# Performance work log

Measured on AMD Instinct MI355X. Metric: run time of the kernel, lower is better.

## Reference

```python
import jax, jax.numpy as jnp
import numpy as np

HIDDEN = 4096
N_HEADS = 32
N_KV_HEADS = 8
HEAD_DIM = HIDDEN // N_HEADS  # 128
Q_SIZE = N_HEADS * HEAD_DIM
KV_SIZE = N_KV_HEADS * HEAD_DIM
ROPE_THETA = 10000.0
EPS = 1e-5
SCALE = HEAD_DIM ** -0.5


def _headwise_layernorm(x, weight, eps):
    # x: [B,S,H,D], weight: [H,D]; LayerNorm over last dim (head_dim), fp32 math
    xf = x.astype(jnp.float32)
    mean = xf.mean(-1, keepdims=True)
    var = jnp.square(xf - mean).mean(-1, keepdims=True)
    y = (xf - mean) * jax.lax.rsqrt(var + eps)
    return (weight.astype(jnp.float32) * y).astype(x.dtype)


def _rope_gptj(x, positions):
    # non-neox (GPT-J) style: rotate interleaved pairs. x: [B,S,H,D]
    half = HEAD_DIM // 2
    inv_freq = 1.0 / (ROPE_THETA ** (jnp.arange(0, HEAD_DIM, 2, dtype=jnp.float32) / HEAD_DIM))
    ang = positions.astype(jnp.float32)[..., None] * inv_freq  # [B,S,half]
    cos = jnp.cos(ang)[:, :, None, :]  # [B,S,1,half]
    sin = jnp.sin(ang)[:, :, None, :]
    x1 = x[..., 0::2]
    x2 = x[..., 1::2]
    o1 = x1 * cos - x2 * sin
    o2 = x2 * cos + x1 * sin
    # re-interleave
    out = jnp.stack([o1, o2], axis=-1).reshape(x.shape)
    return out.astype(x.dtype)


def setup_inputs() -> dict:
    key = jax.random.key(0)
    k1, k2, k3, k4 = jax.random.split(key, 4)
    B, S = 2, 2048
    positions = jnp.tile(jnp.arange(S, dtype=jnp.int32)[None, :], (B, 1))
    hidden_states = jax.random.normal(k1, (B, S, HIDDEN), dtype=jnp.float32)
    Wqkv = jax.random.normal(k2, (HIDDEN, Q_SIZE + 2 * KV_SIZE), dtype=jnp.float32) * (HIDDEN ** -0.5)
    Wo = jax.random.normal(k3, (Q_SIZE, HIDDEN), dtype=jnp.float32) * (Q_SIZE ** -0.5)
    kq, kk = jax.random.split(k4)
    q_norm_w = jnp.ones((N_HEADS, HEAD_DIM), jnp.float32) + 0.02 * jax.random.normal(kq, (N_HEADS, HEAD_DIM))
    k_norm_w = jnp.ones((N_KV_HEADS, HEAD_DIM), jnp.float32) + 0.02 * jax.random.normal(kk, (N_KV_HEADS, HEAD_DIM))
    return {"positions": positions, "hidden_states": hidden_states, "Wqkv": Wqkv,
            "q_norm_w": q_norm_w, "k_norm_w": k_norm_w, "Wo": Wo}


def reference(positions, hidden_states, Wqkv, q_norm_w, k_norm_w, Wo):
    B, S, _ = hidden_states.shape
    qkv = hidden_states @ Wqkv  # [B,S,Q+2KV]
    q, k, v = jnp.split(qkv, [Q_SIZE, Q_SIZE + KV_SIZE], axis=-1)
    q = q.reshape(B, S, N_HEADS, HEAD_DIM)
    k = k.reshape(B, S, N_KV_HEADS, HEAD_DIM)
    v = v.reshape(B, S, N_KV_HEADS, HEAD_DIM)
    # per-head qk-norm
    q = _headwise_layernorm(q, q_norm_w, EPS)
    k = _headwise_layernorm(k, k_norm_w, EPS)
    # non-neox RoPE
    q = _rope_gptj(q, positions)
    k = _rope_gptj(k, positions)
    # GQA: repeat kv heads
    n_rep = N_HEADS // N_KV_HEADS
    k = jnp.repeat(k, n_rep, axis=2)  # [B,S,H,D]
    v = jnp.repeat(v, n_rep, axis=2)
    scores = jnp.einsum('bqhd,bkhd->bhqk', q, k) * SCALE
    causal = jnp.tril(jnp.ones((S, S), dtype=bool))
    scores = jnp.where(causal[None, None], scores, jnp.finfo(scores.dtype).min)
    probs = jax.nn.softmax(scores, axis=-1)
    attn = jnp.einsum('bhqk,bkhd->bqhd', probs, v).reshape(B, S, Q_SIZE)
    return attn @ Wo
```

## Files before the change

kernel.cpp:

```cpp
#include <hip/hip_runtime.h>
#include <hip/hip_bf16.h>
#include <cstdint>

typedef unsigned short u16;
typedef unsigned int u32;
typedef __attribute__((ext_vector_type(8))) short bf16x8;
typedef __attribute__((ext_vector_type(4))) float f32x4;
typedef __attribute__((ext_vector_type(16))) float f32x16;
typedef __attribute__((ext_vector_type(4))) unsigned int u32x4;

#define HIDDEN 4096
#define NH 32
#define NKV 8
#define HD 128
#define QSZ 4096
#define KVSZ 1024
#define QKV_N 6144
#define SEQ 2048
#define NB 2
#define NTOK (NB*SEQ)
#define ATT_SCALE 0.08838834764831845f
#define LOG2E 1.4426950408889634f
#define LN_EPS 1e-5f
#define THRD 12.0f

__device__ __forceinline__ u16 f2bf(float f) {
  union { float f; u32 u; } a; a.f = f;
  u32 r = a.u + 0x7fffu + ((a.u >> 16) & 1u);
  return (u16)(r >> 16);
}
__device__ __forceinline__ float bf2f(u16 h) {
  union { u32 u; float f; } a; a.u = ((u32)h) << 16;
  return a.f;
}

__device__ __forceinline__ void gload_lds16(const void* g, void* l) {
  __builtin_amdgcn_global_load_lds(
      (const __attribute__((address_space(1))) void*)g,
      (__attribute__((address_space(3))) void*)l,
      16, 0, 0);
}

__global__ __launch_bounds__(256)
void conv_f32_bf16(const float* __restrict__ in, u16* __restrict__ out, int n8) {
  int i = blockIdx.x * 256 + threadIdx.x;
  if (i >= n8) return;
  const float4* p = (const float4*)in + (size_t)i * 2;
  float4 v0 = p[0], v1 = p[1];
  u32x4 o;
  o.x = (u32)f2bf(v0.x) | ((u32)f2bf(v0.y) << 16);
  o.y = (u32)f2bf(v0.z) | ((u32)f2bf(v0.w) << 16);
  o.z = (u32)f2bf(v1.x) | ((u32)f2bf(v1.y) << 16);
  o.w = (u32)f2bf(v1.z) | ((u32)f2bf(v1.w) << 16);
  ((u32x4*)out)[i] = o;
}

__global__ __launch_bounds__(256)
void transp_f32_bf16(const float* __restrict__ in, u16* __restrict__ out, int R, int C) {
  __shared__ float tile[32][33];
  int c0 = blockIdx.x << 5, r0 = blockIdx.y << 5;
  int tx = threadIdx.x & 31, ty = threadIdx.x >> 5;
  #pragma unroll
  for (int j = 0; j < 32; j += 8)
    tile[ty + j][tx] = in[(long)(r0 + ty + j) * C + c0 + tx];
  __syncthreads();
  #pragma unroll
  for (int j = 0; j < 32; j += 8)
    out[(long)(c0 + ty + j) * R + r0 + tx] = f2bf(tile[tx][ty + j]);
}

template<typename OutT>
__global__ __launch_bounds__(512, 2)
void gemm_bt6(const u16* __restrict__ A, const u16* __restrict__ Bt,
              OutT* __restrict__ C, int N, int K) {
  extern __shared__ char smem[];
  const int t = threadIdx.x;
  const int lane = t & 63, w = t >> 6;
  const int wr = w >> 2, wc = w & 3;
  const int l31 = lane & 31, l7 = lane & 7, g2 = lane >> 5;
  const int bm = blockIdx.y, bn = blockIdx.x;

  const int ciA0 = t, ciA1 = t + 512;
  const u16* AgS0 = A + (long)(bm * 128 + (ciA0 >> 3)) * K + (((ciA0 & 7) ^ ((ciA0 >> 3) & 7)) << 3);
  const u16* AgS1 = A + (long)(bm * 128 + (ciA1 >> 3)) * K + (((ciA1 & 7) ^ ((ciA1 >> 3) & 7)) << 3);
  const u16* BgS0;
  const u16* BgS1;
  const u16* BgS2;
  const u16* BgS3;
  {
    int ci0 = t, ci1 = t + 512, ci2 = t + 1024, ci3 = t + 1536;
    BgS0 = Bt + (long)(bn * 256 + (ci0 >> 3)) * K + (((ci0 & 7) ^ ((ci0 >> 3) & 7)) << 3);
    BgS1 = Bt + (long)(bn * 256 + (ci1 >> 3)) * K + (((ci1 & 7) ^ ((ci1 >> 3) & 7)) << 3);
    BgS2 = Bt + (long)(bn * 256 + (ci2 >> 3)) * K + (((ci2 & 7) ^ ((ci2 >> 3) & 7)) << 3);
    BgS3 = Bt + (long)(bn * 256 + (ci3 >> 3)) * K + (((ci3 & 7) ^ ((ci3 >> 3) & 7)) << 3);
  }
  const int dA0 = (w * 64) * 16;
  const int dA1 = (512 + w * 64) * 16;
  const int dB0 = 16384 + (w * 64) * 16;
  const int dB1 = 16384 + (512 + w * 64) * 16;
  const int dB2 = 16384 + (1024 + w * 64) * 16;
  const int dB3 = 16384 + (1536 + w * 64) * 16;

  const int arow0 = (wr * 64 + l31) * 128;
  const int brow0 = 16384 + (wc * 64 + l31) * 128;

  f32x16 acc[2][2];
  #pragma unroll
  for (int i = 0; i < 2; ++i)
    #pragma unroll
    for (int j = 0; j < 2; ++j)
      #pragma unroll
      for (int r = 0; r < 16; ++r) acc[i][j][r] = 0.f;

  const int nt = K >> 6;
  char* cbase = smem;
  char* nbase = smem + 49152;
  char* sbase = smem + 98304;

  #define STAGE6(dst, koff) { \
    gload_lds16(AgS0 + (koff), dst + dA0);  gload_lds16(AgS1 + (koff), dst + dA1); \
    gload_lds16(BgS0 + (koff), dst + dB0);  gload_lds16(BgS1 + (koff), dst + dB1); \
    gload_lds16(BgS2 + (koff), dst + dB2);  gload_lds16(BgS3 + (koff), dst + dB3); }

  STAGE6(cbase, 0);
  STAGE6(nbase, 64);
  asm volatile("s_waitcnt vmcnt(6)" ::: "memory");
  __builtin_amdgcn_s_barrier();
  __builtin_amdgcn_sched_barrier(0);

  #define READ_KK(dst, kkv) { \
    const int pcb = (((kkv) * 2 + g2) ^ l7) * 16; \
    dst[0] = *(const bf16x8*)(cbase + arow0 + pcb); \
    dst[1] = *(const bf16x8*)(cbase + arow0 + 32 * 128 + pcb); \
    dst[2] = *(const bf16x8*)(cbase + brow0 + pcb); \
    dst[3] = *(const bf16x8*)(cbase + brow0 + 32 * 128 + pcb); }
  #define MFMA_KK(f) { \
    __builtin_amdgcn_s_setprio(1); \
    acc[0][0] = __builtin_amdgcn_mfma_f32_32x32x16_bf16(f[0], f[2], acc[0][0], 0, 0, 0); \
    acc[0][1] = __builtin_amdgcn_mfma_f32_32x32x16_bf16(f[0], f[3], acc[0][1], 0, 0, 0); \
    acc[1][0] = __builtin_amdgcn_mfma_f32_32x32x16_bf16(f[1], f[2], acc[1][0], 0, 0, 0); \
    acc[1][1] = __builtin_amdgcn_mfma_f32_32x32x16_bf16(f[1], f[3], acc[1][1], 0, 0, 0); \
    __builtin_amdgcn_s_setprio(0); }

  for (int tt = 0; tt < nt; ++tt) {
    const long sk = (long)((tt + 2 < nt) ? (tt + 2) : (nt - 1)) * 64;
    STAGE6(sbase, sk);
    bf16x8 fA[4], fB[4], fC[4], fD[4];
    READ_KK(fA, 0);
    READ_KK(fB, 1);
    MFMA_KK(fA);
    READ_KK(fC, 2);
    MFMA_KK(fB);
    READ_KK(fD, 3);
    MFMA_KK(fC);
    MFMA_KK(fD);
    asm volatile("s_waitcnt vmcnt(6)" ::: "memory");
    __builtin_amdgcn_s_barrier();
    __builtin_amdgcn_sched_barrier(0);
    char* tmp = cbase; cbase = nbase; nbase = sbase; sbase = tmp;
  }
  #undef READ_KK
  #undef MFMA_KK
  #undef STAGE6

  #pragma unroll
  for (int mf = 0; mf < 2; ++mf)
    #pragma unroll
    for (int nf = 0; nf < 2; ++nf)
      #pragma unroll
      for (int r = 0; r < 16; ++r) {
        long row = bm * 128 + wr * 64 + mf * 32 + (r & 3) + 8 * (r >> 2) + 4 * g2;
        long col = bn * 256 + wc * 64 + nf * 32 + l31;
        float v = acc[mf][nf][r];
        if constexpr (sizeof(OutT) == 2) C[row * N + col] = f2bf(v);
        else                             C[row * N + col] = v;
      }
}

__device__ __forceinline__ void ln_rope_head(const u16* __restrict__ src,
                                             const float* __restrict__ wgt,
                                             u16* __restrict__ dst,
                                             int lane, float sa, float ca, float scale) {
  u32 xr = *(const u32*)(src + 2 * lane);
  float x1 = bf2f((u16)(xr & 0xffffu)), x2 = bf2f((u16)(xr >> 16));
  float ssum = x1 + x2;
  #pragma unroll
  for (int off = 1; off < 64; off <<= 1) ssum += __shfl_xor(ssum, off);
  float mean = ssum * (1.0f / 128.0f);
  float e1 = x1 - mean, e2 = x2 - mean;
  float vv = e1 * e1 + e2 * e2;
  #pragma unroll
  for (int off = 1; off < 64; off <<= 1) vv += __shfl_xor(vv, off);
  float rstd = rsqrtf(vv * (1.0f / 128.0f) + LN_EPS);
  float y1 = e1 * rstd * wgt[2 * lane];
  float y2 = e2 * rstd * wgt[2 * lane + 1];
  float o1 = (y1 * ca - y2 * sa) * scale;
  float o2 = (y2 * ca + y1 * sa) * scale;
  *(u32*)(dst + 2 * lane) = (u32)f2bf(o1) | ((u32)f2bf(o2) << 16);
}

__global__ __launch_bounds__(512)
void ln_rope(const u16* __restrict__ qkv, const int* __restrict__ pos,
             const float* __restrict__ qw, const float* __restrict__ kw,
             u16* __restrict__ qo, u16* __restrict__ ko) {
  const int s = blockIdx.x, b = blockIdx.y;
  const int t = threadIdx.x, lane = t & 63, w = t >> 6;
  const long base = (long)(b * SEQ + s) * QKV_N;
  const int p = pos[b * SEQ + s];
  const float expo = (float)(2 * lane) * (1.0f / 128.0f);
  const float inv_freq = exp2f(-expo * 13.287712379549449f);
  float sa, ca;
  sincosf((float)p * inv_freq, &sa, &ca);
  #pragma unroll
  for (int hh = 0; hh < 4; ++hh) {
    int h = w + hh * 8;
    ln_rope_head(qkv + base + h * HD, qw + h * HD,
                 qo + (((long)b * NH + h) * SEQ + s) * HD, lane, sa, ca,
                 ATT_SCALE * LOG2E);
  }
  ln_rope_head(qkv + base + QSZ + w * HD, kw + w * HD,
               ko + (((long)b * NKV + w) * SEQ + s) * HD, lane, sa, ca, 1.0f);
}

__global__ __launch_bounds__(256)
void v_transp(const u16* __restrict__ qkv, u16* __restrict__ vt) {
  __shared__ u16 tile[32][33];
  int s0 = blockIdx.x * 32, d0 = blockIdx.y * 32;
  int bk = blockIdx.z;
  int b = bk >> 3, kvh = bk & 7;
  int tx = threadIdx.x & 31, ty = threadIdx.x >> 5;
  const u16* src = qkv + ((long)(b * SEQ) + s0) * QKV_N + QSZ + KVSZ + kvh * HD + d0;
  #pragma unroll
  for (int j = 0; j < 32; j += 8)
    tile[ty + j][tx] = src[(long)(ty + j) * QKV_N + tx];
  __syncthreads();
  u16* dst = vt + (((long)bk) * HD + d0) * SEQ + s0;
  #pragma unroll
  for (int j = 0; j < 32; j += 8)
    dst[(long)(ty + j) * SEQ + tx] = tile[tx][ty + j];
}

__global__ __launch_bounds__(512, 2)
void flash_attn2(const u16* __restrict__ Qg, const u16* __restrict__ Kg,
                 const u16* __restrict__ Vtg, u16* __restrict__ Og) {
  const int lin = blockIdx.x;
  const int b = lin >> 8;
  const int rem = lin & 255;
  const int h = rem >> 3;
  const int q3 = rem & 7;
  const int qt = b ? (7 - q3) : q3;
  const int kvh = h >> 2;
  const int t = threadIdx.x, lane = t & 63, w = t >> 6;
  const int hh = lane >> 5, l31 = lane & 31;
  const int wq0 = qt * 256 + w * 32;
  const int q = wq0 + l31;

  __shared__ u16 Klds[2][64 * 128];
  __shared__ u16 Vlds[2][128 * 64];

  const u16* Qbase = Qg + (((long)b * NH + h) * SEQ + q) * HD + hh * 8;
  bf16x8 qf[8];
  #pragma unroll
  for (int ks = 0; ks < 8; ++ks) qf[ks] = *(const bf16x8*)(Qbase + ks * 16);

  f32x16 o[4];
  #pragma unroll
  for (int i = 0; i < 4; ++i)
    #pragma unroll
    for (int r = 0; r < 16; ++r) o[i][r] = 0.f;
  float m = -1e30f, l = 0.f;

  const u16* Kbase = Kg + ((long)b * NKV + kvh) * (long)SEQ * HD;
  const u16* Vtbase = Vtg + ((long)b * NKV + kvh) * (long)HD * SEQ;
  const int nt = qt * 4 + 4;

  auto STAGE = [&](int buf, int kt) {
    const int kv0 = kt * 64;
    #pragma unroll
    for (int i = 0; i < 2; ++i) {
      int c = t + i * 512;
      int kv = c >> 4, cc = c & 15;
      int cl = (cc & 8) | ((cc ^ kv) & 7);
      gload_lds16(Kbase + (long)(kv0 + kv) * HD + cl * 8,
                  (char*)(&Klds[buf][0]) + (i * 512 + w * 64) * 16);
    }
    #pragma unroll
    for (int i = 0; i < 2; ++i) {
      int c = t + i * 512;
      int d = c >> 3, cc = c & 7;
      int cl = cc ^ (d & 7);
      gload_lds16(Vtbase + (long)d * SEQ + kv0 + cl * 8,
                  (char*)(&Vlds[buf][0]) + (i * 512 + w * 64) * 16);
    }
  };

  STAGE(0, 0);
  __syncthreads();
  int cur = 0;
  for (int kt = 0; kt < nt; ++kt) {
    const int kv0 = kt * 64;
    if (kt + 1 < nt) STAGE(cur ^ 1, kt + 1);
    if (kv0 <= wq0 + 31) {
      const char* Kb = (const char*)(&Klds[cur][0]);
      const char* Vb = (const char*)(&Vlds[cur][0]);
      f32x16 st[2];
      #pragma unroll
      for (int tt = 0; tt < 2; ++tt)
        #pragma unroll
        for (int r = 0; r < 16; ++r) st[tt][r] = 0.f;
      __builtin_amdgcn_s_setprio(1);
      #pragma unroll
      for (int tt = 0; tt < 2; ++tt) {
        if (kv0 + tt * 32 <= wq0 + 31) {
          #pragma unroll
          for (int ks = 0; ks < 8; ++ks) {
            int ch = ks * 2 + hh;
            int pc = (ch & 8) | ((ch ^ l31) & 7);
            bf16x8 kf = *(const bf16x8*)(Kb + (tt * 32 + l31) * 256 + pc * 16);
            st[tt] = __builtin_amdgcn_mfma_f32_32x32x16_bf16(kf, qf[ks], st[tt], 0, 0, 0);
          }
        }
      }
      __builtin_amdgcn_s_setprio(0);
      if (kv0 + 63 > wq0) {
        #pragma unroll
        for (int tt = 0; tt < 2; ++tt)
          #pragma unroll
          for (int r = 0; r < 16; ++r) {
            int kva = kv0 + tt * 32 + (r & 3) + 8 * (r >> 2) + 4 * hh;
            if (kva > q) st[tt][r] = -1e30f;
          }
      }
      float p0 = -1e30f, p1 = -1e30f, p2 = -1e30f, p3 = -1e30f;
      #pragma unroll
      for (int tt = 0; tt < 2; ++tt)
        #pragma unroll
        for (int r = 0; r < 16; r += 4) {
          p0 = fmaxf(p0, st[tt][r]);
          p1 = fmaxf(p1, st[tt][r + 1]);
          p2 = fmaxf(p2, st[tt][r + 2]);
          p3 = fmaxf(p3, st[tt][r + 3]);
        }
      float mx = fmaxf(fmaxf(p0, p1), fmaxf(p2, p3));
      mx = fmaxf(mx, __shfl_xor(mx, 32));
      if (!__all(mx - m <= THRD)) {
        float mn = fmaxf(m, mx);
        float sc = exp2f(m - mn);
        m = mn;
        float scr[16];
        #pragma unroll
        for (int r = 0; r < 16; ++r)
          scr[r] = __shfl(sc, (r & 3) + 8 * (r >> 2) + 4 * hh);
        #pragma unroll
        for (int db = 0; db < 4; ++db)
          #pragma unroll
          for (int r = 0; r < 16; ++r) o[db][r] *= scr[r];
        l *= sc;
      }
      float s0 = 0.f, s1 = 0.f, s2 = 0.f, s3 = 0.f;
      #pragma unroll
      for (int tt = 0; tt < 2; ++tt)
        #pragma unroll
        for (int r = 0; r < 16; r += 4) {
          float e0 = exp2f(st[tt][r] - m);
          float e1 = exp2f(st[tt][r + 1] - m);
          float e2 = exp2f(st[tt][r + 2] - m);
          float e3 = exp2f(st[tt][r + 3] - m);
          st[tt][r] = e0; st[tt][r + 1] = e1; st[tt][r + 2] = e2; st[tt][r + 3] = e3;
          s0 += e0; s1 += e1; s2 += e2; s3 += e3;
        }
      float rs = (s0 + s1) + (s2 + s3);
      rs += __shfl_xor(rs, 32);
      l += rs;
      bf16x8 pa[4];
      #pragma unroll
      for (int k4 = 0; k4 < 4; ++k4) {
        int s8 = (k4 & 1) * 8, tt = k4 >> 1;
        u32 x0 = (u32)f2bf(st[tt][s8 + 0]) | ((u32)f2bf(st[tt][s8 + 1]) << 16);
        u32 x1 = (u32)f2bf(st[tt][s8 + 2]) | ((u32)f2bf(st[tt][s8 + 3]) << 16);
        u32 y0 = (u32)f2bf(st[tt][s8 + 4]) | ((u32)f2bf(st[tt][s8 + 5]) << 16);
        u32 y1 = (u32)f2bf(st[tt][s8 + 6]) | ((u32)f2bf(st[tt][s8 + 7]) << 16);
        u32 x0s = (u32)__shfl_xor((int)x0, 32), x1s = (u32)__shfl_xor((int)x1, 32);
        u32 y0s = (u32)__shfl_xor((int)y0, 32), y1s = (u32)__shfl_xor((int)y1, 32);
        union { u32 u[4]; bf16x8 v; } pk;
        pk.u[0] = hh ? y0s : x0;
        pk.u[1] = hh ? y1s : x1;
        pk.u[2] = hh ? y0 : x0s;
        pk.u[3] = hh ? y1 : x1s;
        pa[k4] = pk.v;
      }
      __builtin_amdgcn_s_setprio(1);
      #pragma unroll
      for (int k4 = 0; k4 < 4; ++k4)
        #pragma unroll
        for (int db = 0; db < 4; ++db) {
          int ch = k4 * 2 + hh;
          int pcc = ch ^ (l31 & 7);
          bf16x8 vf = *(const bf16x8*)(Vb + (db * 32 + l31) * 128 + pcc * 16);
          o[db] = __builtin_amdgcn_mfma_f32_32x32x16_bf16(pa[k4], vf, o[db], 0, 0, 0);
        }
      __builtin_amdgcn_s_setprio(0);
    }
    __syncthreads();
    cur ^= 1;
  }
  float linv = 1.0f / l;
  float li[16];
  #pragma unroll
  for (int r = 0; r < 16; ++r)
    li[r] = __shfl(linv, (r & 3) + 8 * (r >> 2) + 4 * hh);
  #pragma unroll
  for (int db = 0; db < 4; ++db)
    #pragma unroll
    for (int r = 0; r < 16; ++r) {
      int qr = wq0 + (r & 3) + 8 * (r >> 2) + 4 * hh;
      Og[((long)b * SEQ + qr) * QSZ + h * HD + db * 32 + l31] = f2bf(o[db][r] * li[r]);
    }
}

extern "C" void kernel_launch(void* const* d_in, const int* in_sizes, int n_in,
                              void* d_out, int out_size, void* d_ws, size_t ws_size,
                              hipStream_t stream) {
  const int*   positions = (const int*)d_in[0];
  const float* hidden    = (const float*)d_in[1];
  const float* Wqkv      = (const float*)d_in[2];
  const float* qnw       = (const float*)d_in[3];
  const float* knw       = (const float*)d_in[4];
  const float* Wo        = (const float*)d_in[5];
  float* out = (float*)d_out;
  char* ws = (char*)d_ws;
  const size_t MB = 1024 * 1024;
  u16* hbf   = (u16*)(ws + 0);
  u16* WqkvT = (u16*)(ws + 32 * MB);
  u16* qkvb  = (u16*)(ws + 80 * MB);
  u16* q_arr = (u16*)(ws + 0);
  u16* k_arr = (u16*)(ws + 32 * MB);
  u16* vt_arr= (u16*)(ws + 40 * MB);
  u16* WoT   = (u16*)(ws + 48 * MB);
  u16* Oarr  = (u16*)(ws + 80 * MB);

  const int GEMM_LDS = 3 * 49152;
  (void)hipFuncSetAttribute((const void*)&gemm_bt6<u16>,
        hipFuncAttributeMaxDynamicSharedMemorySize, GEMM_LDS);
  (void)hipFuncSetAttribute((const void*)&gemm_bt6<float>,
        hipFuncAttributeMaxDynamicSharedMemorySize, GEMM_LDS);

  conv_f32_bf16<<<dim3(NTOK * HIDDEN / 8 / 256), 256, 0, stream>>>(hidden, hbf, NTOK * HIDDEN / 8);
  transp_f32_bf16<<<dim3(QKV_N / 32, HIDDEN / 32), 256, 0, stream>>>(Wqkv, WqkvT, HIDDEN, QKV_N);
  gemm_bt6<u16><<<dim3(QKV_N / 256, NTOK / 128), 512, GEMM_LDS, stream>>>(hbf, WqkvT, qkvb, QKV_N, HIDDEN);
  ln_rope<<<dim3(SEQ, NB), 512, 0, stream>>>(qkvb, positions, qnw, knw, q_arr, k_arr);
  v_transp<<<dim3(SEQ / 32, HD / 32, NB * NKV), 256, 0, stream>>>(qkvb, vt_arr);
  transp_f32_bf16<<<dim3(HIDDEN / 32, QSZ / 32), 256, 0, stream>>>(Wo, WoT, QSZ, HIDDEN);
  flash_attn2<<<dim3(512), 512, 0, stream>>>(q_arr, k_arr, vt_arr, Oarr);
  gemm_bt6<float><<<dim3(HIDDEN / 256, NTOK / 128), 512, GEMM_LDS, stream>>>(Oarr, WoT, out, HIDDEN, QSZ);
}
```

Baseline: 584.7 us.

## Halve GEMM K-step for higher occupancy and pair causal query tiles in attention

```diff
diff --git a/kernel.cpp b/kernel.cpp
--- a/kernel.cpp
+++ b/kernel.cpp
@@ -70,39 +70,33 @@
 }
 
 template<typename OutT>
-__global__ __launch_bounds__(512, 2)
-void gemm_bt6(const u16* __restrict__ A, const u16* __restrict__ Bt,
+__global__ __launch_bounds__(512, 4)
+void gemm_bt9(const u16* __restrict__ A, const u16* __restrict__ Bt,
               OutT* __restrict__ C, int N, int K) {
   extern __shared__ char smem[];
   const int t = threadIdx.x;
   const int lane = t & 63, w = t >> 6;
   const int wr = w >> 2, wc = w & 3;
-  const int l31 = lane & 31, l7 = lane & 7, g2 = lane >> 5;
+  const int l31 = lane & 31, g2 = lane >> 5;
   const int bm = blockIdx.y, bn = blockIdx.x;
 
-  const int ciA0 = t, ciA1 = t + 512;
-  const u16* AgS0 = A + (long)(bm * 128 + (ciA0 >> 3)) * K + (((ciA0 & 7) ^ ((ciA0 >> 3) & 7)) << 3);
-  const u16* AgS1 = A + (long)(bm * 128 + (ciA1 >> 3)) * K + (((ciA1 & 7) ^ ((ciA1 >> 3) & 7)) << 3);
-  const u16* BgS0;
-  const u16* BgS1;
-  const u16* BgS2;
-  const u16* BgS3;
+  const u16* pA;  const u16* pB0;  const u16* pB1;
   {
-    int ci0 = t, ci1 = t + 512, ci2 = t + 1024, ci3 = t + 1536;
-    BgS0 = Bt + (long)(bn * 256 + (ci0 >> 3)) * K + (((ci0 & 7) ^ ((ci0 >> 3) & 7)) << 3);
-    BgS1 = Bt + (long)(bn * 256 + (ci1 >> 3)) * K + (((ci1 & 7) ^ ((ci1 >> 3) & 7)) << 3);
-    BgS2 = Bt + (long)(bn * 256 + (ci2 >> 3)) * K + (((ci2 & 7) ^ ((ci2 >> 3) & 7)) << 3);
-    BgS3 = Bt + (long)(bn * 256 + (ci3 >> 3)) * K + (((ci3 & 7) ^ ((ci3 >> 3) & 7)) << 3);
+    int ci = t;
+    int line = ci >> 3, phys = ci & 7;
+    int lg = phys ^ (line & 7);
+    pA = A + (long)(bm * 128 + 2 * line + (lg >> 2)) * K + ((lg & 3) << 3);
+    ci = t;
+    line = ci >> 3; phys = ci & 7; lg = phys ^ (line & 7);
+    pB0 = Bt + (long)(bn * 256 + 2 * line + (lg >> 2)) * K + ((lg & 3) << 3);
+    ci = t + 512;
+    line = ci >> 3; phys = ci & 7; lg = phys ^ (line & 7);
+    pB1 = Bt + (long)(bn * 256 + 2 * line + (lg >> 2)) * K + ((lg & 3) << 3);
   }
-  const int dA0 = (w * 64) * 16;
-  const int dA1 = (512 + w * 64) * 16;
-  const int dB0 = 16384 + (w * 64) * 16;
-  const int dB1 = 16384 + (512 + w * 64) * 16;
-  const int dB2 = 16384 + (1024 + w * 64) * 16;
-  const int dB3 = 16384 + (1536 + w * 64) * 16;
-
-  const int arow0 = (wr * 64 + l31) * 128;
-  const int brow0 = 16384 + (wc * 64 + l31) * 128;
+  const int dS = w * 1024;
+
+  const int lhalf = l31 >> 1;
+  const int lgbase = (l31 & 1) * 4 + g2;
 
   f32x16 acc[2][2];
   #pragma unroll
@@ -112,29 +106,33 @@
       #pragma unroll
       for (int r = 0; r < 16; ++r) acc[i][j][r] = 0.f;
 
-  const int nt = K >> 6;
+  const int nt = K >> 5;
   char* cbase = smem;
-  char* nbase = smem + 49152;
-  char* sbase = smem + 98304;
-
-  #define STAGE6(dst, koff) { \
-    gload_lds16(AgS0 + (koff), dst + dA0);  gload_lds16(AgS1 + (koff), dst + dA1); \
-    gload_lds16(BgS0 + (koff), dst + dB0);  gload_lds16(BgS1 + (koff), dst + dB1); \
-    gload_lds16(BgS2 + (koff), dst + dB2);  gload_lds16(BgS3 + (koff), dst + dB3); }
-
-  STAGE6(cbase, 0);
-  STAGE6(nbase, 64);
-  asm volatile("s_waitcnt vmcnt(6)" ::: "memory");
+  char* nbase = smem + 24576;
+  char* sbase = smem + 49152;
+
+  #define STAGE9(dst, koff) { \
+    gload_lds16(pA  + (koff), (dst) + dS); \
+    gload_lds16(pB0 + (koff), (dst) + 8192 + dS); \
+    gload_lds16(pB1 + (koff), (dst) + 16384 + dS); }
+
+  STAGE9(cbase, 0);
+  STAGE9(nbase, 32);
+  asm volatile("s_waitcnt vmcnt(3)" ::: "memory");
   __builtin_amdgcn_s_barrier();
   __builtin_amdgcn_sched_barrier(0);
 
-  #define READ_KK(dst, kkv) { \
-    const int pcb = (((kkv) * 2 + g2) ^ l7) * 16; \
-    dst[0] = *(const bf16x8*)(cbase + arow0 + pcb); \
-    dst[1] = *(const bf16x8*)(cbase + arow0 + 32 * 128 + pcb); \
-    dst[2] = *(const bf16x8*)(cbase + brow0 + pcb); \
-    dst[3] = *(const bf16x8*)(cbase + brow0 + 32 * 128 + pcb); }
-  #define MFMA_KK(f) { \
+  #define READ9(dst, s) { \
+    const int lg_ = lgbase + (s) * 2; \
+    { int ln_ = wr * 32 + lhalf;          int ph_ = lg_ ^ (ln_ & 7); \
+      dst[0] = *(const bf16x8*)(cbase + ln_ * 128 + ph_ * 16); } \
+    { int ln_ = wr * 32 + 16 + lhalf;     int ph_ = lg_ ^ (ln_ & 7); \
+      dst[1] = *(const bf16x8*)(cbase + ln_ * 128 + ph_ * 16); } \
+    { int ln_ = wc * 32 + lhalf;          int ph_ = lg_ ^ (ln_ & 7); \
+      dst[2] = *(const bf16x8*)(cbase + 8192 + ln_ * 128 + ph_ * 16); } \
+    { int ln_ = wc * 32 + 16 + lhalf;     int ph_ = lg_ ^ (ln_ & 7); \
+      dst[3] = *(const bf16x8*)(cbase + 8192 + ln_ * 128 + ph_ * 16); } }
+  #define MFMA9(f) { \
     __builtin_amdgcn_s_setprio(1); \
     acc[0][0] = __builtin_amdgcn_mfma_f32_32x32x16_bf16(f[0], f[2], acc[0][0], 0, 0, 0); \
     acc[0][1] = __builtin_amdgcn_mfma_f32_32x32x16_bf16(f[0], f[3], acc[0][1], 0, 0, 0); \
@@ -143,25 +141,21 @@
     __builtin_amdgcn_s_setprio(0); }
 
   for (int tt = 0; tt < nt; ++tt) {
-    const long sk = (long)((tt + 2 < nt) ? (tt + 2) : (nt - 1)) * 64;
-    STAGE6(sbase, sk);
-    bf16x8 fA[4], fB[4], fC[4], fD[4];
-    READ_KK(fA, 0);
-    READ_KK(fB, 1);
-    MFMA_KK(fA);
-    READ_KK(fC, 2);
-    MFMA_KK(fB);
-    READ_KK(fD, 3);
-    MFMA_KK(fC);
-    MFMA_KK(fD);
-    asm volatile("s_waitcnt vmcnt(6)" ::: "memory");
+    const long sk = (long)((tt + 2 < nt) ? (tt + 2) : (nt - 1)) * 32;
+    bf16x8 f0[4], f1[4];
+    READ9(f0, 0);
+    READ9(f1, 1);
+    STAGE9(sbase, sk);
+    MFMA9(f0);
+    MFMA9(f1);
+    asm volatile("s_waitcnt vmcnt(3)" ::: "memory");
     __builtin_amdgcn_s_barrier();
     __builtin_amdgcn_sched_barrier(0);
     char* tmp = cbase; cbase = nbase; nbase = sbase; sbase = tmp;
   }
-  #undef READ_KK
-  #undef MFMA_KK
-  #undef STAGE6
+  #undef READ9
+  #undef MFMA9
+  #undef STAGE9
 
   #pragma unroll
   for (int mf = 0; mf < 2; ++mf)
@@ -241,38 +235,22 @@
 }
 
 __global__ __launch_bounds__(512, 2)
-void flash_attn2(const u16* __restrict__ Qg, const u16* __restrict__ Kg,
+void flash_attn3(const u16* __restrict__ Qg, const u16* __restrict__ Kg,
                  const u16* __restrict__ Vtg, u16* __restrict__ Og) {
   const int lin = blockIdx.x;
-  const int b = lin >> 8;
-  const int rem = lin & 255;
-  const int h = rem >> 3;
-  const int q3 = rem & 7;
-  const int qt = b ? (7 - q3) : q3;
+  const int b = lin >> 7;
+  const int rem = lin & 127;
+  const int h = rem >> 2;
+  const int qp = rem & 3;
   const int kvh = h >> 2;
   const int t = threadIdx.x, lane = t & 63, w = t >> 6;
   const int hh = lane >> 5, l31 = lane & 31;
-  const int wq0 = qt * 256 + w * 32;
-  const int q = wq0 + l31;
 
   __shared__ u16 Klds[2][64 * 128];
   __shared__ u16 Vlds[2][128 * 64];
 
-  const u16* Qbase = Qg + (((long)b * NH + h) * SEQ + q) * HD + hh * 8;
-  bf16x8 qf[8];
-  #pragma unroll
-  for (int ks = 0; ks < 8; ++ks) qf[ks] = *(const bf16x8*)(Qbase + ks * 16);
-
-  f32x16 o[4];
-  #pragma unroll
-  for (int i = 0; i < 4; ++i)
-    #pragma unroll
-    for (int r = 0; r < 16; ++r) o[i][r] = 0.f;
-  float m = -1e30f, l = 0.f;
-
   const u16* Kbase = Kg + ((long)b * NKV + kvh) * (long)SEQ * HD;
   const u16* Vtbase = Vtg + ((long)b * NKV + kvh) * (long)HD * SEQ;
-  const int nt = qt * 4 + 4;
 
   auto STAGE = [&](int buf, int kt) {
     const int kv0 = kt * 64;
@@ -294,128 +272,147 @@
     }
   };
 
-  STAGE(0, 0);
-  __syncthreads();
-  int cur = 0;
-  for (int kt = 0; kt < nt; ++kt) {
-    const int kv0 = kt * 64;
-    if (kt + 1 < nt) STAGE(cur ^ 1, kt + 1);
-    if (kv0 <= wq0 + 31) {
-      const char* Kb = (const char*)(&Klds[cur][0]);
-      const char* Vb = (const char*)(&Vlds[cur][0]);
-      f32x16 st[2];
+  for (int seg = 0; seg < 2; ++seg) {
+    const int qt = seg ? qp : (7 - qp);
+    const int wq0 = qt * 256 + w * 32;
+    const int q = wq0 + l31;
+    const u16* Qbase = Qg + (((long)b * NH + h) * SEQ + q) * HD + hh * 8;
+    bf16x8 qf[8];
+    #pragma unroll
+    for (int ks = 0; ks < 8; ++ks) qf[ks] = *(const bf16x8*)(Qbase + ks * 16);
+
+    f32x16 o[4];
+    #pragma unroll
+    for (int i = 0; i < 4; ++i)
       #pragma unroll
-      for (int tt = 0; tt < 2; ++tt)
-        #pragma unroll
-        for (int r = 0; r < 16; ++r) st[tt][r] = 0.f;
-      __builtin_amdgcn_s_setprio(1);
-      #pragma unroll
-      for (int tt = 0; tt < 2; ++tt) {
-        if (kv0 + tt * 32 <= wq0 + 31) {
-          #pragma unroll
-          for (int ks = 0; ks < 8; ++ks) {
-            int ch = ks * 2 + hh;
-            int pc = (ch & 8) | ((ch ^ l31) & 7);
-            bf16x8 kf = *(const bf16x8*)(Kb + (tt * 32 + l31) * 256 + pc * 16);
-            st[tt] = __builtin_amdgcn_mfma_f32_32x32x16_bf16(kf, qf[ks], st[tt], 0, 0, 0);
+      for (int r = 0; r < 16; ++r) o[i][r] = 0.f;
+    float m = -1e30f, l = 0.f;
+    const int nt = qt * 4 + 4;
+
+    __syncthreads();
+    STAGE(0, 0);
+    __syncthreads();
+    int cur = 0;
+    for (int kt = 0; kt < nt; ++kt) {
+      const int kv0 = kt * 64;
+      if (kt + 1 < nt) STAGE(cur ^ 1, kt + 1);
+      if (kv0 <= wq0 + 31) {
+        const char* Kb = (const char*)(&Klds[cur][0]);
+        const char* Vb = (const char*)(&Vlds[cur][0]);
+        f32x16 st[2];
+        #pragma unroll
+        for (int tt = 0; tt < 2; ++tt)
+          #pragma unroll
+          for (int r = 0; r < 16; ++r) st[tt][r] = 0.f;
+        __builtin_amdgcn_s_setprio(1);
+        #pragma unroll
+        for (int tt = 0; tt < 2; ++tt) {
+          if (kv0 + tt * 32 <= wq0 + 31) {
+            #pragma unroll
+            for (int ks = 0; ks < 8; ++ks) {
+              int ch = ks * 2 + hh;
+              int pc = (ch & 8) | ((ch ^ l31) & 7);
+              bf16x8 kf = *(const bf16x8*)(Kb + (tt * 32 + l31) * 256 + pc * 16);
+              st[tt] = __builtin_amdgcn_mfma_f32_32x32x16_bf16(kf, qf[ks], st[tt], 0, 0, 0);
+            }
           }
         }
+        __builtin_amdgcn_s_setprio(0);
+        if (kv0 + 63 > wq0) {
+          #pragma unroll
+          for (int tt = 0; tt < 2; ++tt)
+            #pragma unroll
+            for (int r = 0; r < 16; ++r) {
+              int kva = kv0 + tt * 32 + (r & 3) + 8 * (r >> 2) + 4 * hh;
+              if (kva > q) st[tt][r] = -1e30f;
+            }
+        }
+        float p0 = -1e30f, p1 = -1e30f, p2 = -1e30f, p3 = -1e30f;
+        #pragma unroll
+        for (int tt = 0; tt < 2; ++tt)
+          #pragma unroll
+          for (int r = 0; r < 16; r += 4) {
+            p0 = fmaxf(p0, st[tt][r]);
+            p1 = fmaxf(p1, st[tt][r + 1]);
+            p2 = fmaxf(p2, st[tt][r + 2]);
+            p3 = fmaxf(p3, st[tt][r + 3]);
+          }
+        float mx = fmaxf(fmaxf(p0, p1), fmaxf(p2, p3));
+        mx = fmaxf(mx, __shfl_xor(mx, 32));
+        if (!__all(mx - m <= THRD)) {
+          float mn = fmaxf(m, mx);
+          float sc = exp2f(m - mn);
+          m = mn;
+          float scr[16];
+          #pragma unroll
+          for (int r = 0; r < 16; ++r)
+            scr[r] = __shfl(sc, (r & 3) + 8 * (r >> 2) + 4 * hh);
+          #pragma unroll
+          for (int db = 0; db < 4; ++db)
+            #pragma unroll
+            for (int r = 0; r < 16; ++r) o[db][r] *= scr[r];
+          l *= sc;
+        }
+        float s0 = 0.f, s1 = 0.f, s2 = 0.f, s3 = 0.f;
+        #pragma unroll
+        for (int tt = 0; tt < 2; ++tt)
+          #pragma unroll
+          for (int r = 0; r < 16; r += 4) {
+            float e0 = exp2f(st[tt][r] - m);
+            float e1 = exp2f(st[tt][r + 1] - m);
+            float e2 = exp2f(st[tt][r + 2] - m);
+            float e3 = exp2f(st[tt][r + 3] - m);
+            st[tt][r] = e0; st[tt][r + 1] = e1; st[tt][r + 2] = e2; st[tt][r + 3] = e3;
+            s0 += e0; s1 += e1; s2 += e2; s3 += e3;
+          }
+        float rs = (s0 + s1) + (s2 + s3);
+        rs += __shfl_xor(rs, 32);
+        l += rs;
+        bf16x8 pa[4];
+        #pragma unroll
+        for (int k4 = 0; k4 < 4; ++k4) {
+          int s8 = (k4 & 1) * 8, tt = k4 >> 1;
+          u32 x0 = (u32)f2bf(st[tt][s8 + 0]) | ((u32)f2bf(st[tt][s8 + 1]) << 16);
+          u32 x1 = (u32)f2bf(st[tt][s8 + 2]) | ((u32)f2bf(st[tt][s8 + 3]) << 16);
+          u32 y0 = (u32)f2bf(st[tt][s8 + 4]) | ((u32)f2bf(st[tt][s8 + 5]) << 16);
+          u32 y1 = (u32)f2bf(st[tt][s8 + 6]) | ((u32)f2bf(st[tt][s8 + 7]) << 16);
+          u32 x0s = (u32)__shfl_xor((int)x0, 32), x1s = (u32)__shfl_xor((int)x1, 32);
+          u32 y0s = (u32)__shfl_xor((int)y0, 32), y1s = (u32)__shfl_xor((int)y1, 32);
+          union { u32 u[4]; bf16x8 v; } pk;
+          pk.u[0] = hh ? y0s : x0;
+          pk.u[1] = hh ? y1s : x1;
+          pk.u[2] = hh ? y0 : x0s;
+          pk.u[3] = hh ? y1 : x1s;
+          pa[k4] = pk.v;
+        }
+        __builtin_amdgcn_s_setprio(1);
+        #pragma unroll
+        for (int k4 = 0; k4 < 4; ++k4)
+          #pragma unroll
+          for (int db = 0; db < 4; ++db) {
+            int ch = k4 * 2 + hh;
+            int pcc = ch ^ (l31 & 7);
+            bf16x8 vf = *(const bf16x8*)(Vb + (db * 32 + l31) * 128 + pcc * 16);
+            o[db] = __builtin_amdgcn_mfma_f32_32x32x16_bf16(pa[k4], vf, o[db], 0, 0, 0);
+          }
+        __builtin_amdgcn_s_setprio(0);
       }
-      __builtin_amdgcn_s_setprio(0);
-      if (kv0 + 63 > wq0) {
-        #pragma unroll
-        for (int tt = 0; tt < 2; ++tt)
-          #pragma unroll
-          for (int r = 0; r < 16; ++r) {
-            int kva = kv0 + tt * 32 + (r & 3) + 8 * (r >> 2) + 4 * hh;
-            if (kva > q) st[tt][r] = -1e30f;
-          }
+      __syncthreads();
+      cur ^= 1;
+    }
+    float linv = 1.0f / l;
+    float li[16];
+    #pragma unroll
+    for (int r = 0; r < 16; ++r)
+      li[r] = __shfl(linv, (r & 3) + 8 * (r >> 2) + 4 * hh);
+    #pragma unroll
+    for (int db = 0; db < 4; ++db)
+      #pragma unroll
+      for (int r = 0; r < 16; ++r) {
+        int qr = wq0 + (r & 3) + 8 * (r >> 2) + 4 * hh;
+        Og[((long)b * SEQ + qr) * QSZ + h * HD + db * 32 + l31] = f2bf(o[db][r] * li[r]);
       }
-      float p0 = -1e30f, p1 = -1e30f, p2 = -1e30f, p3 = -1e30f;
-      #pragma unroll
-      for (int tt = 0; tt < 2; ++tt)
-        #pragma unroll
-        for (int r = 0; r < 16; r += 4) {
-          p0 = fmaxf(p0, st[tt][r]);
-          p1 = fmaxf(p1, st[tt][r + 1]);
-          p2 = fmaxf(p2, st[tt][r + 2]);
-          p3 = fmaxf(p3, st[tt][r + 3]);
-        }
-      float mx = fmaxf(fmaxf(p0, p1), fmaxf(p2, p3));
-      mx = fmaxf(mx, __shfl_xor(mx, 32));
-      if (!__all(mx - m <= THRD)) {
-        float mn = fmaxf(m, mx);
-        float sc = exp2f(m - mn);
-        m = mn;
-        float scr[16];
-        #pragma unroll
-        for (int r = 0; r < 16; ++r)
-          scr[r] = __shfl(sc, (r & 3) + 8 * (r >> 2) + 4 * hh);
-        #pragma unroll
-        for (int db = 0; db < 4; ++db)
-          #pragma unroll
-          for (int r = 0; r < 16; ++r) o[db][r] *= scr[r];
-        l *= sc;
-      }
-      float s0 = 0.f, s1 = 0.f, s2 = 0.f, s3 = 0.f;
-      #pragma unroll
-      for (int tt = 0; tt < 2; ++tt)
-        #pragma unroll
-        for (int r = 0; r < 16; r += 4) {
-          float e0 = exp2f(st[tt][r] - m);
-          float e1 = exp2f(st[tt][r + 1] - m);
-          float e2 = exp2f(st[tt][r + 2] - m);
-          float e3 = exp2f(st[tt][r + 3] - m);
-          st[tt][r] = e0; st[tt][r + 1] = e1; st[tt][r + 2] = e2; st[tt][r + 3] = e3;
-          s0 += e0; s1 += e1; s2 += e2; s3 += e3;
-        }
-      float rs = (s0 + s1) + (s2 + s3);
-      rs += __shfl_xor(rs, 32);
-      l += rs;
-      bf16x8 pa[4];
-      #pragma unroll
-      for (int k4 = 0; k4 < 4; ++k4) {
-        int s8 = (k4 & 1) * 8, tt = k4 >> 1;
-        u32 x0 = (u32)f2bf(st[tt][s8 + 0]) | ((u32)f2bf(st[tt][s8 + 1]) << 16);
-        u32 x1 = (u32)f2bf(st[tt][s8 + 2]) | ((u32)f2bf(st[tt][s8 + 3]) << 16);
-        u32 y0 = (u32)f2bf(st[tt][s8 + 4]) | ((u32)f2bf(st[tt][s8 + 5]) << 16);
-        u32 y1 = (u32)f2bf(st[tt][s8 + 6]) | ((u32)f2bf(st[tt][s8 + 7]) << 16);
-        u32 x0s = (u32)__shfl_xor((int)x0, 32), x1s = (u32)__shfl_xor((int)x1, 32);
-        u32 y0s = (u32)__shfl_xor((int)y0, 32), y1s = (u32)__shfl_xor((int)y1, 32);
-        union { u32 u[4]; bf16x8 v; } pk;
-        pk.u[0] = hh ? y0s : x0;
-        pk.u[1] = hh ? y1s : x1;
-        pk.u[2] = hh ? y0 : x0s;
-        pk.u[3] = hh ? y1 : x1s;
-        pa[k4] = pk.v;
-      }
-      __builtin_amdgcn_s_setprio(1);
-      #pragma unroll
-      for (int k4 = 0; k4 < 4; ++k4)
-        #pragma unroll
-        for (int db = 0; db < 4; ++db) {
-          int ch = k4 * 2 + hh;
-          int pcc = ch ^ (l31 & 7);
-          bf16x8 vf = *(const bf16x8*)(Vb + (db * 32 + l31) * 128 + pcc * 16);
-          o[db] = __builtin_amdgcn_mfma_f32_32x32x16_bf16(pa[k4], vf, o[db], 0, 0, 0);
-        }
-      __builtin_amdgcn_s_setprio(0);
-    }
-    __syncthreads();
-    cur ^= 1;
   }
-  float linv = 1.0f / l;
-  float li[16];
-  #pragma unroll
-  for (int r = 0; r < 16; ++r)
-    li[r] = __shfl(linv, (r & 3) + 8 * (r >> 2) + 4 * hh);
-  #pragma unroll
-  for (int db = 0; db < 4; ++db)
-    #pragma unroll
-    for (int r = 0; r < 16; ++r) {
-      int qr = wq0 + (r & 3) + 8 * (r >> 2) + 4 * hh;
-      Og[((long)b * SEQ + qr) * QSZ + h * HD + db * 32 + l31] = f2bf(o[db][r] * li[r]);
-    }
 }
 
 extern "C" void kernel_launch(void* const* d_in, const int* in_sizes, int n_in,
@@ -439,18 +436,18 @@
   u16* WoT   = (u16*)(ws + 48 * MB);
   u16* Oarr  = (u16*)(ws + 80 * MB);
 
-  const int GEMM_LDS = 3 * 49152;
-  (void)hipFuncSetAttribute((const void*)&gemm_bt6<u16>,
+  const int GEMM_LDS = 3 * 24576;
+  (void)hipFuncSetAttribute((const void*)&gemm_bt9<u16>,
         hipFuncAttributeMaxDynamicSharedMemorySize, GEMM_LDS);
-  (void)hipFuncSetAttribute((const void*)&gemm_bt6<float>,
+  (void)hipFuncSetAttribute((const void*)&gemm_bt9<float>,
         hipFuncAttributeMaxDynamicSharedMemorySize, GEMM_LDS);
 
   conv_f32_bf16<<<dim3(NTOK * HIDDEN / 8 / 256), 256, 0, stream>>>(hidden, hbf, NTOK * HIDDEN / 8);
   transp_f32_bf16<<<dim3(QKV_N / 32, HIDDEN / 32), 256, 0, stream>>>(Wqkv, WqkvT, HIDDEN, QKV_N);
-  gemm_bt6<u16><<<dim3(QKV_N / 256, NTOK / 128), 512, GEMM_LDS, stream>>>(hbf, WqkvT, qkvb, QKV_N, HIDDEN);
+  gemm_bt9<u16><<<dim3(QKV_N / 256, NTOK / 128), 512, GEMM_LDS, stream>>>(hbf, WqkvT, qkvb, QKV_N, HIDDEN);
   ln_rope<<<dim3(SEQ, NB), 512, 0, stream>>>(qkvb, positions, qnw, knw, q_arr, k_arr);
   v_transp<<<dim3(SEQ / 32, HD / 32, NB * NKV), 256, 0, stream>>>(qkvb, vt_arr);
   transp_f32_bf16<<<dim3(HIDDEN / 32, QSZ / 32), 256, 0, stream>>>(Wo, WoT, QSZ, HIDDEN);
-  flash_attn2<<<dim3(512), 512, 0, stream>>>(q_arr, k_arr, vt_arr, Oarr);
-  gemm_bt6<float><<<dim3(HIDDEN / 256, NTOK / 128), 512, GEMM_LDS, stream>>>(Oarr, WoT, out, HIDDEN, QSZ);
-}
+  flash_attn3<<<dim3(256), 512, 0, stream>>>(q_arr, k_arr, vt_arr, Oarr);
+  gemm_bt9<float><<<dim3(HIDDEN / 256, NTOK / 128), 512, GEMM_LDS, stream>>>(Oarr, WoT, out, HIDDEN, QSZ);
+}
```

Result: slower. 598.6 us (+2.4%).
